# Kernel tuning notes

Measured on AMD Instinct MI355X. Metric: run time of the kernel, lower is better.

The kernel has to match this reference:

```python
import math
import jax, jax.numpy as jnp
import numpy as np

B, L, D = 8, 512, 512          # batch, seq, d_model
G, S = 8, 4                    # n_groups, expert_scale (clones per group)
FG, FE = 4, 64                 # features per group, d_feat_emb
E = G * S                      # n_experts = 32
DH, RH = 256, 256              # d_expert_hidden, d_router_hidden
TEMP, SHARP, BIAS = 1.0, 16.0, 1.0
GK, SK = 2, 2                  # group_top_k, expert_top_k


def setup_inputs() -> dict:
    key = jax.random.key(0)
    ks = jax.random.split(key, 12)
    def n(k, shape, fan_in):
        return (jax.random.normal(k, shape) * (fan_in ** -0.5)).astype(jnp.float32)
    return {
        "hidden": jax.random.normal(ks[0], (B, L, D), jnp.float32),
        "feat": jax.random.uniform(ks[1], (B, L, G * FG), dtype=jnp.float32),
        "valid_mask": jnp.ones((B, L), jnp.bool_),
        # outer (group) router: hidden -> RH -> G
        "Wr1": n(ks[2], (D, RH), D), "br1": jnp.zeros((RH,), jnp.float32),
        "Wr2": n(ks[3], (RH, G), RH), "br2": jnp.zeros((G,), jnp.float32),
        # per-group feature embedding: FG -> FE
        "Wfe": n(ks[4], (G, FG, FE), FG), "bfe": jnp.zeros((G, FE), jnp.float32),
        # per-group inner (clone) router on [hidden ; feat_emb] -> S
        "Win_h": n(ks[5], (G, D, S), D + FE),
        "Win_f": n(ks[6], (G, FE, S), D + FE),
        "bin_b": jnp.zeros((G, S), jnp.float32),
        # per-expert MLP: D -> DH -> D
        "We1": n(ks[7], (E, D, DH), D), "be1": jnp.zeros((E, DH), jnp.float32),
        "We2": n(ks[8], (E, DH, D), DH), "be2": jnp.zeros((E, D), jnp.float32),
    }


def _to_ratio(x):
    # faithful to _to_ratio: clamp if already in [0,1], else Gaussian CDF
    clamped = jnp.clip(x, 0.0, 1.0)
    cdf = jnp.clip(0.5 * (1.0 + jax.lax.erf(x / math.sqrt(2.0))), 0.0, 1.0)
    in01 = jnp.logical_and(x.min() >= -1e-6, x.max() <= 1.0 + 1e-6)
    return jnp.where(in01, clamped, cdf)


def _topk_softmax(logits, k):
    # softmax over top-k entries, zeros elsewhere (== scatter of softmax(top_vals))
    vals, _ = jax.lax.top_k(logits, k)
    thresh = vals[..., -1:]
    neg = jnp.finfo(logits.dtype).min
    return jax.nn.softmax(jnp.where(logits >= thresh, logits, neg), axis=-1)


def _forward(hidden, feat, Wr1, br1, Wr2, br2, Wfe, bfe, Win_h, Win_f, bin_b,
             We1, be1, We2, be2):
    gelu = lambda x: jax.nn.gelu(x, approximate=False)  # torch nn.GELU default
    # ---- outer (group) router: hidden-only, token mode ----
    gh = gelu(hidden @ Wr1 + br1)                       # [B,L,RH]
    glog = (gh @ Wr2 + br2) / TEMP                      # [B,L,G]
    gw = _topk_softmax(glog, GK)                        # [B,L,G]
    # ---- inner rule teacher: bins over normalized group feature ratios ----
    feat_g = feat.reshape(B, L, G, FG)
    score = _to_ratio(feat_g).mean(-1, keepdims=True)   # [B,L,G,1]
    centers = jnp.linspace(0.0, 1.0, S, dtype=jnp.float32)
    rule = -SHARP * (score - centers) ** 2              # [B,L,G,S]
    # ---- inner (clone) router: hidden + group feature embedding + rule bias ----
    femb = jnp.einsum('blgf,gfe->blge', feat_g, Wfe) + bfe          # [B,L,G,FE]
    ilog = (jnp.einsum('bld,gds->blgs', hidden, Win_h)
            + jnp.einsum('blge,ges->blgs', femb, Win_f)
            + bin_b + BIAS * rule) / TEMP                            # [B,L,G,S]
    cw = _topk_softmax(ilog, SK)                                     # [B,L,G,S]
    # ---- combine hierarchical weights (group-major expert order) ----
    w = (gw[..., None] * cw).reshape(B, L, E)                        # [B,L,E]
    # ---- dense grouped expert MLPs (dropout=0 at eval) ----
    h1 = gelu(jnp.einsum('bld,edh->bleh', hidden, We1) + be1)        # [B,L,E,DH]
    y = jnp.einsum('bleh,ehd,ble->bld', h1, We2, w)
    y = y + jnp.einsum('ble,ed->bld', w, be2)
    return y


def reference(hidden, feat, valid_mask, Wr1, br1, Wr2, br2, Wfe, bfe,
              Win_h, Win_f, bin_b, We1, be1, We2, be2):
    del valid_mask  # token-mode routing; mask only used for session pooling
    return _forward(hidden, feat, Wr1, br1, Wr2, br2, Wfe, bfe,
                    Win_h, Win_f, bin_b, We1, be1, We2, be2)
```

## Files before the change

### kernel.cpp

```cpp
#include <hip/hip_runtime.h>
#include <hip/hip_bf16.h>
#include <math.h>

#define BB   8
#define LL   512
#define DD   512
#define GG   8
#define SSS  4
#define FGC  4
#define FEC  64
#define EEC  32
#define DHC  256
#define RHC  256
#define NT   (BB*LL)
#define TM   32
#define TR   8

#define XC_STRIDE 264
#define CPAD 32
#define EGRID 1024
#define RBLK 512
#define PBLK 4096

typedef __attribute__((ext_vector_type(8))) short short8;
typedef __attribute__((ext_vector_type(4))) float floatx4;

__device__ __forceinline__ float gelu_exact(float x) {
    return 0.5f * x * (1.0f + erff(x * 0.70710678118654752440f));
}

__device__ __forceinline__ unsigned pk2(float a, float b) {
    union { __hip_bfloat162 h; unsigned u; } cv;
    cv.h = __float22bfloat162_rn(make_float2(a, b));
    return cv.u;
}
union U4S8 { unsigned u[4]; short8 s; };

__device__ __forceinline__ floatx4 mfma16(short8 a, short8 b, floatx4 c) {
    return __builtin_amdgcn_mfma_f32_16x16x32_bf16(a, b, c, 0, 0, 0);
}

__global__ __launch_bounds__(256) void prep_kernel(
    const float* __restrict__ Win_h, const float* __restrict__ Win_f,
    const float* __restrict__ Wfe, const float* __restrict__ bfe,
    const float* __restrict__ bin_b,
    float* __restrict__ WinT, float* __restrict__ M2, float* __restrict__ c2b,
    int* __restrict__ counts_zero)
{
    const int tid = threadIdx.x;
    if (blockIdx.x < 64) {
        int idx = blockIdx.x * 256 + tid;
        int d = idx >> 5, gs = idx & 31;
        int g = gs >> 2, s = gs & 3;
        WinT[idx] = Win_h[(size_t)g*DD*SSS + d*SSS + s];
    } else if (blockIdx.x == 64) {
        if (tid < GG*FGC*SSS) {
            int g = tid >> 4, f = (tid >> 2) & 3, s = tid & 3;
            float acc = 0.f;
            for (int e = 0; e < FEC; ++e)
                acc += Wfe[(size_t)g*FGC*FEC + f*FEC + e] * Win_f[(size_t)g*FEC*SSS + e*SSS + s];
            M2[tid] = acc;
        } else if (tid < GG*FGC*SSS + GG*SSS) {
            int gs = tid - GG*FGC*SSS;
            int g = gs >> 2, s = gs & 3;
            float acc = bin_b[gs];
            for (int e = 0; e < FEC; ++e)
                acc += bfe[g*FEC + e] * Win_f[(size_t)g*FEC*SSS + e*SSS + s];
            c2b[gs] = acc;
        }
    } else {
        for (int i = tid; i < EEC*CPAD; i += 256) counts_zero[i] = 0;
    }
}

__global__ __launch_bounds__(256) void route_and_pack(
    const float* __restrict__ hidden, const float* __restrict__ feat,
    const float* __restrict__ Wr1, const float* __restrict__ br1,
    const float* __restrict__ Wr2, const float* __restrict__ br2,
    const float* __restrict__ WinT, const float* __restrict__ M2,
    const float* __restrict__ c2b,
    int* __restrict__ bucket_tok, float* __restrict__ bucket_w,
    int* __restrict__ counts, int* __restrict__ nslot,
    const float* __restrict__ We1, const float* __restrict__ We2,
    short* __restrict__ Wp1, short* __restrict__ Wp2)
{
    const int tid = threadIdx.x;

    if (blockIdx.x >= RBLK) {
        const int gid = (blockIdx.x - RBLK) * 256 + tid;
        if (gid < EEC*16*16*64) {
            const int lane = gid & 63;
            const int nb   = (gid >> 6) & 15;
            const int i    = (gid >> 10) & 15;
            const int e    = gid >> 14;
            const int k0   = i*32 + (lane >> 4)*8;
            const int n    = nb*16 + (lane & 15);
            const float* s = We1 + ((size_t)e*DD + k0)*DHC + n;
            float f[8];
            #pragma unroll
            for (int j = 0; j < 8; ++j) f[j] = s[(size_t)j*DHC];
            U4S8 cv;
            cv.u[0] = pk2(f[0], f[1]); cv.u[1] = pk2(f[2], f[3]);
            cv.u[2] = pk2(f[4], f[5]); cv.u[3] = pk2(f[6], f[7]);
            *(short8*)(Wp1 + (size_t)gid*8) = cv.s;
        } else {
            const int g2   = gid - EEC*16*16*64;
            const int lane = g2 & 63;
            const int nb   = (g2 >> 6) & 31;
            const int i    = (g2 >> 11) & 7;
            const int e    = g2 >> 14;
            const int k0   = i*32 + (lane >> 4)*8;
            const int n    = nb*16 + (lane & 15);
            const float* s = We2 + ((size_t)e*DHC + k0)*DD + n;
            float f[8];
            #pragma unroll
            for (int j = 0; j < 8; ++j) f[j] = s[(size_t)j*DD];
            U4S8 cv;
            cv.u[0] = pk2(f[0], f[1]); cv.u[1] = pk2(f[2], f[3]);
            cv.u[2] = pk2(f[4], f[5]); cv.u[3] = pk2(f[6], f[7]);
            *(short8*)(Wp2 + (size_t)g2*8) = cv.s;
        }
        return;
    }

    const int t0 = blockIdx.x * TR;

    __shared__ float hs[TR][DD];
    __shared__ float ghs[TR][RHC+4];
    __shared__ float featb[TR][GG*FGC];
    __shared__ float glogp[TR][GG][4];
    __shared__ float gwvb[TR][GG];
    __shared__ float scoreb[TR][GG];
    __shared__ float ilogb[TR][GG*SSS];
    __shared__ float cwvb[TR][GG*SSS];

    for (int i = tid; i < TR*DD; i += 256) {
        int r = i >> 9, c = i & 511;
        hs[r][c] = hidden[(size_t)(t0 + r)*DD + c];
    }
    if (tid < TR*GG*FGC) {
        int r = tid >> 5, c = tid & 31;
        featb[r][c] = feat[(t0 + r)*(GG*FGC) + c];
    }
    __syncthreads();

    if (tid < TR*GG) {
        int t = tid >> 3, g = tid & 7;
        float s = 0.f;
        #pragma unroll
        for (int f = 0; f < FGC; ++f) s += fminf(fmaxf(featb[t][g*4+f], 0.f), 1.f);
        scoreb[t][g] = s * 0.25f;
    }

    {
        float acc[TR];
        float b = br1[tid];
        #pragma unroll
        for (int t = 0; t < TR; ++t) acc[t] = b;
        #pragma unroll 4
        for (int k = 0; k < DD; k += 4) {
            float w0 = Wr1[(size_t)k*RHC + tid];
            float w1 = Wr1[(size_t)(k+1)*RHC + tid];
            float w2 = Wr1[(size_t)(k+2)*RHC + tid];
            float w3 = Wr1[(size_t)(k+3)*RHC + tid];
            #pragma unroll
            for (int t = 0; t < TR; ++t) {
                float4 h = *(const float4*)(&hs[t][k]);
                acc[t] += h.x*w0 + h.y*w1 + h.z*w2 + h.w*w3;
            }
        }
        #pragma unroll
        for (int t = 0; t < TR; ++t) ghs[t][tid] = gelu_exact(acc[t]);
    }
    __syncthreads();

    {
        const int t = tid >> 5, g = (tid >> 2) & 7, q = tid & 3;
        float s = (q == 0) ? br2[g] : 0.f;
        const float* wr = Wr2 + g;
        #pragma unroll 4
        for (int h = q*64; h < q*64 + 64; ++h) s += ghs[t][h] * wr[(size_t)h*GG];
        glogp[t][g][q] = s;
    }

    {
        const int t = tid >> 5, gs = tid & 31;
        const int g = gs >> 2, s = gs & 3;
        float acc = 0.f;
        #pragma unroll 8
        for (int k = 0; k < DD; ++k) acc += hs[t][k] * WinT[k*32 + gs];
        const float* m2 = M2 + g*16 + s;
        acc += featb[t][g*4+0]*m2[0] + featb[t][g*4+1]*m2[4]
             + featb[t][g*4+2]*m2[8] + featb[t][g*4+3]*m2[12];
        const float centers[4] = {0.0f, 1.0f/3.0f, 2.0f/3.0f, 1.0f};
        float diff = scoreb[t][g] - centers[s];
        ilogb[t][gs] = acc + c2b[gs] - 16.0f * diff * diff;
    }
    __syncthreads();

    if (tid < TR) {
        int t = tid;
        float gl[GG];
        #pragma unroll
        for (int g = 0; g < GG; ++g)
            gl[g] = glogp[t][g][0] + glogp[t][g][1] + glogp[t][g][2] + glogp[t][g][3];
        float a = -INFINITY, b = -INFINITY;
        #pragma unroll
        for (int g = 0; g < GG; ++g) {
            float v = gl[g];
            if (v > a) { b = a; a = v; } else if (v > b) { b = v; }
        }
        float thresh = b, m = a, sum = 0.f;
        float ex[GG];
        #pragma unroll
        for (int g = 0; g < GG; ++g) {
            ex[g] = (gl[g] >= thresh) ? __expf(gl[g] - m) : 0.f;
            sum += ex[g];
        }
        float inv = 1.0f / sum;
        #pragma unroll
        for (int g = 0; g < GG; ++g) gwvb[t][g] = ex[g] * inv;
    }
    if (tid < TR*GG) {
        int t = tid >> 3, g = tid & 7;
        float vv[4] = {ilogb[t][g*4+0], ilogb[t][g*4+1], ilogb[t][g*4+2], ilogb[t][g*4+3]};
        float a = -INFINITY, b = -INFINITY;
        #pragma unroll
        for (int s = 0; s < 4; ++s) {
            float v = vv[s];
            if (v > a) { b = a; a = v; } else if (v > b) { b = v; }
        }
        float thresh = b, m = a, sum = 0.f;
        float ex[4];
        #pragma unroll
        for (int s = 0; s < 4; ++s) {
            ex[s] = (vv[s] >= thresh) ? __expf(vv[s] - m) : 0.f;
            sum += ex[s];
        }
        float inv = 1.0f / sum;
        #pragma unroll
        for (int s = 0; s < 4; ++s) cwvb[t][g*4 + s] = ex[s] * inv;
    }
    __syncthreads();

    if (tid < TR) {
        int t = tid;
        int a = 0;
        for (int g = 0; g < GG; ++g) {
            float gw = gwvb[t][g];
            if (gw > 0.f) {
                for (int s = 0; s < SSS; ++s) {
                    float w = gw * cwvb[t][g*4 + s];
                    if (w > 0.f && a < 4) {
                        int ee = g*SSS + s;
                        int pos = atomicAdd(&counts[ee*CPAD], 1);
                        bucket_tok[ee*NT + pos] = ((t0 + t) << 2) | a;
                        bucket_w[ee*NT + pos]   = w;
                        ++a;
                    }
                }
            }
        }
        nslot[t0 + t] = a;
    }
}

__global__ __launch_bounds__(256) void expert_mfma7(
    const float* __restrict__ hidden,
    const short* __restrict__ Wp1, const float* __restrict__ be1,
    const short* __restrict__ Wp2, const float* __restrict__ be2,
    const int* __restrict__ bucket_tok, const float* __restrict__ bucket_w,
    const int* __restrict__ counts,
    float* __restrict__ y_part)
{
    const int tid  = threadIdx.x;
    const int wave = tid >> 6;
    const int lane = tid & 63;
    const int lm   = lane & 15;
    const int quad = lane >> 4;

    __shared__ short Xp[64 * XC_STRIDE];
    __shared__ short Hp[32 * XC_STRIDE];
    __shared__ int   toks[TM];
    __shared__ float tws[TM];
    __shared__ int   s_cnt[EEC], s_off[EEC + 1];

    if (tid < EEC) s_cnt[tid] = counts[tid*CPAD];
    __syncthreads();
    if (tid == 0) {
        int acc = 0;
        #pragma unroll
        for (int e = 0; e < EEC; ++e) {
            s_off[e] = acc;
            acc += (s_cnt[e] + TM - 1) / TM;
        }
        s_off[EEC] = acc;
    }
    __syncthreads();
    const int NW = s_off[EEC];

    const int q    = NW >> 3, r = NW & 7;
    const int xcd  = blockIdx.x & 7;
    const int rank = blockIdx.x >> 3;
    const int len  = q + (xcd < r ? 1 : 0);
    const int base = (xcd < r) ? xcd*(q+1) : r*(q+1) + (xcd - r)*q;

    for (int j = rank; j < len; j += (EGRID >> 3)) {
        const int it = base + j;
        int e = 0;
        while (e < EEC - 1 && it >= s_off[e + 1]) ++e;
        const int tile = it - s_off[e];
        const int cnt  = s_cnt[e];
        const int r0   = tile * TM;
        const int nrow = min(TM, cnt - r0);

        const short* W1 = Wp1 + (size_t)e * (16*16*64*8);
        const short* W2 = Wp2 + (size_t)e * (8*32*64*8);

        if (tid < TM) {
            if (tid < nrow) {
                toks[tid] = bucket_tok[e*NT + r0 + tid];
                tws[tid]  = bucket_w[e*NT + r0 + tid];
            } else { toks[tid] = -1; tws[tid] = 0.f; }
        }

        short8 b1c[4];
        {
            const short* wb = W1 + ((size_t)wave*4)*512 + lane*8;
            #pragma unroll
            for (int nb = 0; nb < 4; ++nb) b1c[nb] = *(const short8*)(wb + nb*512);
        }
        __syncthreads();

        {
            const int xr = tid >> 3;
            const int xk = tid & 7;
            const int bt = toks[xr];
            const float* src = hidden + (size_t)(bt < 0 ? 0 : (bt >> 2))*DD;
            #pragma unroll
            for (int i = 0; i < 8; ++i) {
                const int k8 = xk + 8*i;
                float4 v0 = make_float4(0.f,0.f,0.f,0.f), v1 = v0;
                if (bt >= 0) {
                    v0 = *(const float4*)(src + k8*8);
                    v1 = *(const float4*)(src + k8*8 + 4);
                }
                U4S8 cv;
                cv.u[0] = pk2(v0.x, v0.y); cv.u[1] = pk2(v0.z, v0.w);
                cv.u[2] = pk2(v1.x, v1.y); cv.u[3] = pk2(v1.z, v1.w);
                *(short8*)(&Xp[k8 * XC_STRIDE + xr * 8]) = cv.s;
            }
        }
        __syncthreads();

        floatx4 acc[2][4];
        #pragma unroll
        for (int mb = 0; mb < 2; ++mb)
            #pragma unroll
            for (int nb = 0; nb < 4; ++nb)
                acc[mb][nb] = (floatx4){0.f, 0.f, 0.f, 0.f};

        for (int i = 0; i < 16; ++i) {
            const int k8 = i*4 + quad;
            short8 b1n[4];
            if (i < 15) {
                const short* wb = W1 + ((size_t)(i+1)*16 + wave*4)*512 + lane*8;
                #pragma unroll
                for (int nb = 0; nb < 4; ++nb) b1n[nb] = *(const short8*)(wb + nb*512);
            }
            short8 a0 = *(const short8*)(&Xp[k8 * XC_STRIDE + lm * 8]);
            short8 a1 = *(const short8*)(&Xp[k8 * XC_STRIDE + (16 + lm) * 8]);
            #pragma unroll
            for (int nb = 0; nb < 4; ++nb) {
                acc[0][nb] = mfma16(a0, b1c[nb], acc[0][nb]);
                acc[1][nb] = mfma16(a1, b1c[nb], acc[1][nb]);
            }
            if (i < 15) {
                #pragma unroll
                for (int nb = 0; nb < 4; ++nb) b1c[nb] = b1n[nb];
            }
        }

        short8 b2c[8];
        {
            const short* wb = W2 + ((size_t)wave*8)*512 + lane*8;
            #pragma unroll
            for (int nb = 0; nb < 8; ++nb) b2c[nb] = *(const short8*)(wb + nb*512);
        }

        #pragma unroll
        for (int nb = 0; nb < 4; ++nb) {
            const int h = wave*64 + nb*16 + lm;
            const float b1 = be1[e*DHC + h];
            #pragma unroll
            for (int mb = 0; mb < 2; ++mb) {
                #pragma unroll
                for (int r2 = 0; r2 < 4; r2 += 2) {
                    const int m0 = mb*16 + quad*4 + r2;
                    unsigned u = pk2(gelu_exact(acc[mb][nb][r2]   + b1),
                                     gelu_exact(acc[mb][nb][r2+1] + b1));
                    Hp[(h >> 3) * XC_STRIDE + m0 * 8 + (h & 7)]     = (short)(u & 0xffff);
                    Hp[(h >> 3) * XC_STRIDE + (m0+1) * 8 + (h & 7)] = (short)(u >> 16);
                }
            }
        }
        __syncthreads();

        floatx4 c[2][8];
        #pragma unroll
        for (int mb = 0; mb < 2; ++mb)
            #pragma unroll
            for (int nb = 0; nb < 8; ++nb)
                c[mb][nb] = (floatx4){0.f, 0.f, 0.f, 0.f};

        for (int i = 0; i < 8; ++i) {
            const int k8 = i*4 + quad;
            short8 b2n[8];
            if (i < 7) {
                const short* wb = W2 + ((size_t)(i+1)*32 + wave*8)*512 + lane*8;
                #pragma unroll
                for (int nb = 0; nb < 8; ++nb) b2n[nb] = *(const short8*)(wb + nb*512);
            }
            short8 a0 = *(const short8*)(&Hp[k8 * XC_STRIDE + lm * 8]);
            short8 a1 = *(const short8*)(&Hp[k8 * XC_STRIDE + (16 + lm) * 8]);
            #pragma unroll
            for (int nb = 0; nb < 8; ++nb) {
                c[0][nb] = mfma16(a0, b2c[nb], c[0][nb]);
                c[1][nb] = mfma16(a1, b2c[nb], c[1][nb]);
            }
            if (i < 7) {
                #pragma unroll
                for (int nb = 0; nb < 8; ++nb) b2c[nb] = b2n[nb];
            }
        }

        #pragma unroll
        for (int nb = 0; nb < 8; ++nb) {
            const int col = wave*128 + nb*16 + lm;
            const float b2 = be2[e*DD + col];
            #pragma unroll
            for (int mb = 0; mb < 2; ++mb) {
                #pragma unroll
                for (int r2 = 0; r2 < 4; ++r2) {
                    const int m = mb*16 + quad*4 + r2;
                    const int bt = toks[m];
                    if (bt >= 0)
                        y_part[(size_t)bt*DD + col] = tws[m] * (c[mb][nb][r2] + b2);
                }
            }
        }
        __syncthreads();
    }
}

__global__ __launch_bounds__(256) void reduce_y(
    const float* __restrict__ y_part, const int* __restrict__ nslot,
    float* __restrict__ y)
{
    const int idx = blockIdx.x * 256 + threadIdx.x;
    const int t  = idx >> 7;
    const int c4 = idx & 127;
    const int ns = nslot[t];
    float4 s = make_float4(0.f, 0.f, 0.f, 0.f);
    const float* p = y_part + ((size_t)t*4)*DD + c4*4;
    for (int a = 0; a < ns; ++a) {
        float4 v = *(const float4*)(p + (size_t)a*DD);
        s.x += v.x; s.y += v.y; s.z += v.z; s.w += v.w;
    }
    *(float4*)(y + (size_t)t*DD + c4*4) = s;
}

__global__ __launch_bounds__(256) void expert_mfma3(
    const float* __restrict__ hidden,
    const float* __restrict__ We1, const float* __restrict__ be1,
    const float* __restrict__ We2, const float* __restrict__ be2,
    const int* __restrict__ bucket_tok, const float* __restrict__ bucket_w,
    const int* __restrict__ counts,
    float* __restrict__ y)
{
    const int e    = blockIdx.x & 31;
    const int tile = blockIdx.x >> 5;
    const int cnt  = counts[e*CPAD];
    const int r0   = tile * TM;
    if (r0 >= cnt) return;
    const int nrow = min(TM, cnt - r0);
    const int tid  = threadIdx.x;
    const int wave = tid >> 6;
    const int lane = tid & 63;
    const int lm   = lane & 15;
    const int quad = lane >> 4;

    __shared__ short Xp[64 * XC_STRIDE];
    __shared__ short Hp[32 * XC_STRIDE];
    __shared__ int   toks[TM];
    __shared__ float tws[TM];

    if (tid < TM) {
        if (tid < nrow) {
            toks[tid] = bucket_tok[e*NT + r0 + tid] >> 2;
            tws[tid]  = bucket_w[e*NT + r0 + tid];
        } else { toks[tid] = -1; tws[tid] = 0.f; }
    }
    __syncthreads();

    {
        const int xr = tid >> 3;
        const int xk = tid & 7;
        const int tk = toks[xr];
        const float* src = hidden + (size_t)(tk < 0 ? 0 : tk)*DD;
        #pragma unroll
        for (int i = 0; i < 8; ++i) {
            const int k8 = xk + 8*i;
            float4 v0 = make_float4(0.f,0.f,0.f,0.f), v1 = v0;
            if (tk >= 0) {
                v0 = *(const float4*)(src + k8*8);
                v1 = *(const float4*)(src + k8*8 + 4);
            }
            U4S8 cv;
            cv.u[0] = pk2(v0.x, v0.y); cv.u[1] = pk2(v0.z, v0.w);
            cv.u[2] = pk2(v1.x, v1.y); cv.u[3] = pk2(v1.z, v1.w);
            *(short8*)(&Xp[k8 * XC_STRIDE + xr * 8]) = cv.s;
        }
    }
    __syncthreads();

    floatx4 acc[2][4];
    #pragma unroll
    for (int mb = 0; mb < 2; ++mb)
        #pragma unroll
        for (int nb = 0; nb < 4; ++nb)
            acc[mb][nb] = (floatx4){0.f, 0.f, 0.f, 0.f};

    const float* W1 = We1 + (size_t)e * DD * DHC;

    for (int i = 0; i < 16; ++i) {
        const int k8 = i*4 + quad;
        short8 a0 = *(const short8*)(&Xp[k8 * XC_STRIDE + lm * 8]);
        short8 a1 = *(const short8*)(&Xp[k8 * XC_STRIDE + (16 + lm) * 8]);
        float wreg[4][8];
        #pragma unroll
        for (int nb = 0; nb < 4; ++nb) {
            const float* s = W1 + (size_t)(k8*8)*DHC + wave*64 + nb*16 + lm;
            #pragma unroll
            for (int j = 0; j < 8; ++j) wreg[nb][j] = s[(size_t)j*DHC];
        }
        #pragma unroll
        for (int nb = 0; nb < 4; ++nb) {
            U4S8 cv;
            cv.u[0] = pk2(wreg[nb][0], wreg[nb][1]);
            cv.u[1] = pk2(wreg[nb][2], wreg[nb][3]);
            cv.u[2] = pk2(wreg[nb][4], wreg[nb][5]);
            cv.u[3] = pk2(wreg[nb][6], wreg[nb][7]);
            acc[0][nb] = mfma16(a0, cv.s, acc[0][nb]);
            acc[1][nb] = mfma16(a1, cv.s, acc[1][nb]);
        }
    }

    #pragma unroll
    for (int nb = 0; nb < 4; ++nb) {
        const int h = wave*64 + nb*16 + lm;
        const float b1 = be1[e*DHC + h];
        #pragma unroll
        for (int mb = 0; mb < 2; ++mb) {
            #pragma unroll
            for (int r = 0; r < 4; r += 2) {
                const int m0 = mb*16 + quad*4 + r;
                unsigned u = pk2(gelu_exact(acc[mb][nb][r]   + b1),
                                 gelu_exact(acc[mb][nb][r+1] + b1));
                Hp[(h >> 3) * XC_STRIDE + m0 * 8 + (h & 7)]     = (short)(u & 0xffff);
                Hp[(h >> 3) * XC_STRIDE + (m0+1) * 8 + (h & 7)] = (short)(u >> 16);
            }
        }
    }
    __syncthreads();

    floatx4 c[2][8];
    #pragma unroll
    for (int mb = 0; mb < 2; ++mb)
        #pragma unroll
        for (int nb = 0; nb < 8; ++nb)
            c[mb][nb] = (floatx4){0.f, 0.f, 0.f, 0.f};

    const float* W2 = We2 + (size_t)e * DHC * DD;

    for (int i = 0; i < 8; ++i) {
        const int k8 = i*4 + quad;
        short8 a0 = *(const short8*)(&Hp[k8 * XC_STRIDE + lm * 8]);
        short8 a1 = *(const short8*)(&Hp[k8 * XC_STRIDE + (16 + lm) * 8]);
        #pragma unroll
        for (int half = 0; half < 2; ++half) {
            float wreg[4][8];
            #pragma unroll
            for (int nb4 = 0; nb4 < 4; ++nb4) {
                const int n = wave*128 + (half*4 + nb4)*16 + lm;
                const float* s = W2 + (size_t)(k8*8)*DD + n;
                #pragma unroll
                for (int j = 0; j < 8; ++j) wreg[nb4][j] = s[(size_t)j*DD];
            }
            #pragma unroll
            for (int nb4 = 0; nb4 < 4; ++nb4) {
                const int nb = half*4 + nb4;
                U4S8 cv;
                cv.u[0] = pk2(wreg[nb4][0], wreg[nb4][1]);
                cv.u[1] = pk2(wreg[nb4][2], wreg[nb4][3]);
                cv.u[2] = pk2(wreg[nb4][4], wreg[nb4][5]);
                cv.u[3] = pk2(wreg[nb4][6], wreg[nb4][7]);
                c[0][nb] = mfma16(a0, cv.s, c[0][nb]);
                c[1][nb] = mfma16(a1, cv.s, c[1][nb]);
            }
        }
    }

    #pragma unroll
    for (int nb = 0; nb < 8; ++nb) {
        const int col = wave*128 + nb*16 + lm;
        const float b2 = be2[e*DD + col];
        #pragma unroll
        for (int mb = 0; mb < 2; ++mb) {
            #pragma unroll
            for (int r = 0; r < 4; ++r) {
                const int m = mb*16 + quad*4 + r;
                const int tk = toks[m];
                if (tk >= 0)
                    atomicAdd(&y[(size_t)tk*DD + col], tws[m] * (c[mb][nb][r] + b2));
            }
        }
    }
}

extern "C" void kernel_launch(void* const* d_in, const int* in_sizes, int n_in,
                              void* d_out, int out_size, void* d_ws, size_t ws_size,
                              hipStream_t stream) {
    const float* hidden = (const float*)d_in[0];
    const float* feat   = (const float*)d_in[1];
    const float* Wr1    = (const float*)d_in[3];
    const float* br1    = (const float*)d_in[4];
    const float* Wr2    = (const float*)d_in[5];
    const float* br2    = (const float*)d_in[6];
    const float* Wfe    = (const float*)d_in[7];
    const float* bfe    = (const float*)d_in[8];
    const float* Win_h  = (const float*)d_in[9];
    const float* Win_f  = (const float*)d_in[10];
    const float* bin_b  = (const float*)d_in[11];
    const float* We1    = (const float*)d_in[12];
    const float* be1    = (const float*)d_in[13];
    const float* We2    = (const float*)d_in[14];
    const float* be2    = (const float*)d_in[15];
    float* y = (float*)d_out;

    char* ws = (char*)d_ws;
    int*   bucket_tok = (int*)ws;    ws += (size_t)EEC*NT*sizeof(int);
    float* bucket_w   = (float*)ws;  ws += (size_t)EEC*NT*sizeof(float);
    int*   counts     = (int*)ws;    ws += (size_t)EEC*CPAD*sizeof(int);
    float* WinT       = (float*)ws;  ws += (size_t)DD*EEC*sizeof(float);
    float* M2         = (float*)ws;  ws += 512;
    float* c2b        = (float*)ws;  ws += 256;
    int*   nslot      = (int*)ws;    ws += (size_t)NT*sizeof(int);
    size_t base_used  = (size_t)(ws - (char*)d_ws);

    short* Wp1    = (short*)ws;
    short* Wp2    = Wp1 + (size_t)EEC*DD*DHC;
    float* y_part = (float*)(Wp2 + (size_t)EEC*DHC*DD);
    size_t need_fast = base_used
                     + 2*(size_t)EEC*DD*DHC*sizeof(short)
                     + (size_t)NT*4*DD*sizeof(float);
    const bool fast = (ws_size >= need_fast);

    prep_kernel<<<66, 256, 0, stream>>>(Win_h, Win_f, Wfe, bfe, bin_b,
                                        WinT, M2, c2b, counts);

    if (fast) {
        route_and_pack<<<RBLK + PBLK, 256, 0, stream>>>(
            hidden, feat, Wr1, br1, Wr2, br2, WinT, M2, c2b,
            bucket_tok, bucket_w, counts, nslot,
            We1, We2, Wp1, Wp2);

        expert_mfma7<<<EGRID, 256, 0, stream>>>(hidden, Wp1, be1, Wp2, be2,
                                                bucket_tok, bucket_w, counts,
                                                y_part);

        reduce_y<<<(NT*DD/4)/256, 256, 0, stream>>>(y_part, nslot, y);
    } else {
        hipMemsetAsync(y, 0, (size_t)NT*DD*sizeof(float), stream);

        route_and_pack<<<RBLK, 256, 0, stream>>>(
            hidden, feat, Wr1, br1, Wr2, br2, WinT, M2, c2b,
            bucket_tok, bucket_w, counts, nslot,
            We1, We2, (short*)nullptr, (short*)nullptr);

        expert_mfma3<<<(NT/TM)*EEC, 256, 0, stream>>>(hidden, We1, be1, We2, be2,
                                                      bucket_tok, bucket_w, counts, y);
    }
}
```

Before: 250.0 us.

## Fuse per-token partial reduction into expert kernel via completion counters

Removes the separate reduce_y launch. Each expert tile bumps a per-token atomic counter after writing its partial outputs, and the block that finishes a token's last slot sums that token's partials into y. The counter array sits right after counts, so the prep kernel now zeroes it alongside counts. This saves a launch and a full pass over y_part, at the cost of extra atomics, thread fences and serialized reduction work inside the expert blocks.

```diff
diff --git a/kernel.cpp b/kernel.cpp
--- a/kernel.cpp
+++ b/kernel.cpp
@@ -69,7 +69,7 @@
             c2b[gs] = acc;
         }
     } else {
-        for (int i = tid; i < EEC*CPAD; i += 256) counts_zero[i] = 0;
+        for (int i = tid; i < EEC*CPAD + NT; i += 256) counts_zero[i] = 0;
     }
 }
 
@@ -265,13 +265,14 @@
     }
 }
 
-__global__ __launch_bounds__(256) void expert_mfma7(
+__global__ __launch_bounds__(256) void expert_mfma8(
     const float* __restrict__ hidden,
     const short* __restrict__ Wp1, const float* __restrict__ be1,
     const short* __restrict__ Wp2, const float* __restrict__ be2,
     const int* __restrict__ bucket_tok, const float* __restrict__ bucket_w,
-    const int* __restrict__ counts,
-    float* __restrict__ y_part)
+    const int* __restrict__ counts, const int* __restrict__ nslot,
+    int* __restrict__ tokdone,
+    float* __restrict__ y_part, float* __restrict__ y)
 {
     const int tid  = threadIdx.x;
     const int wave = tid >> 6;
@@ -283,6 +284,7 @@
     __shared__ short Hp[32 * XC_STRIDE];
     __shared__ int   toks[TM];
     __shared__ float tws[TM];
+    __shared__ int   red_tok[TM];
     __shared__ int   s_cnt[EEC], s_off[EEC + 1];
 
     if (tid < EEC) s_cnt[tid] = counts[tid*CPAD];
@@ -449,25 +451,38 @@
                 }
             }
         }
+
         __syncthreads();
-    }
-}
-
-__global__ __launch_bounds__(256) void reduce_y(
-    const float* __restrict__ y_part, const int* __restrict__ nslot,
-    float* __restrict__ y)
-{
-    const int idx = blockIdx.x * 256 + threadIdx.x;
-    const int t  = idx >> 7;
-    const int c4 = idx & 127;
-    const int ns = nslot[t];
-    float4 s = make_float4(0.f, 0.f, 0.f, 0.f);
-    const float* p = y_part + ((size_t)t*4)*DD + c4*4;
-    for (int a = 0; a < ns; ++a) {
-        float4 v = *(const float4*)(p + (size_t)a*DD);
-        s.x += v.x; s.y += v.y; s.z += v.z; s.w += v.w;
-    }
-    *(float4*)(y + (size_t)t*DD + c4*4) = s;
+        __threadfence();
+        __syncthreads();
+        if (tid < TM) {
+            int flag = -1;
+            const int bt = toks[tid];
+            if (bt >= 0) {
+                const int t  = bt >> 2;
+                const int ns = nslot[t];
+                if (atomicAdd(&tokdone[t], 1) == ns - 1) flag = t;
+            }
+            red_tok[tid] = flag;
+        }
+        __syncthreads();
+        __threadfence();
+        for (int m = 0; m < TM; ++m) {
+            const int t = red_tok[m];
+            if (t < 0) continue;
+            const int ns = nslot[t];
+            if (tid < 128) {
+                const float* p = y_part + ((size_t)t*4)*DD + tid*4;
+                float4 s = make_float4(0.f, 0.f, 0.f, 0.f);
+                for (int a = 0; a < ns; ++a) {
+                    float4 v = *(const float4*)(p + (size_t)a*DD);
+                    s.x += v.x; s.y += v.y; s.z += v.z; s.w += v.w;
+                }
+                *(float4*)(y + (size_t)t*DD + tid*4) = s;
+            }
+        }
+        __syncthreads();
+    }
 }
 
 __global__ __launch_bounds__(256) void expert_mfma3(
@@ -652,6 +667,7 @@
     int*   bucket_tok = (int*)ws;    ws += (size_t)EEC*NT*sizeof(int);
     float* bucket_w   = (float*)ws;  ws += (size_t)EEC*NT*sizeof(float);
     int*   counts     = (int*)ws;    ws += (size_t)EEC*CPAD*sizeof(int);
+    int*   tokdone    = (int*)ws;    ws += (size_t)NT*sizeof(int);
     float* WinT       = (float*)ws;  ws += (size_t)DD*EEC*sizeof(float);
     float* M2         = (float*)ws;  ws += 512;
     float* c2b        = (float*)ws;  ws += 256;
@@ -675,11 +691,9 @@
             bucket_tok, bucket_w, counts, nslot,
             We1, We2, Wp1, Wp2);
 
-        expert_mfma7<<<EGRID, 256, 0, stream>>>(hidden, Wp1, be1, Wp2, be2,
+        expert_mfma8<<<EGRID, 256, 0, stream>>>(hidden, Wp1, be1, Wp2, be2,
                                                 bucket_tok, bucket_w, counts,
-                                                y_part);
-
-        reduce_y<<<(NT*DD/4)/256, 256, 0, stream>>>(y_part, nslot, y);
+                                                nslot, tokdone, y_part, y);
     } else {
         hipMemsetAsync(y, 0, (size_t)NT*DD*sizeof(float), stream);
 
```

After: 378.5 us. 1.51x slower.
